# Kernel optimization log

Hardware: AMD Instinct MI355X
Metric: run time of the kernel (lower is better)

The kernel has to match this reference:

```python
import jax, jax.numpy as jnp
import numpy as np

N_NODES = 50000
N_EDGES = 800000
N_GRAPHS = 2500
HIDDEN = 64
IN_DIM = 14  # 11 QM9 features + 3 pos


def setup_inputs() -> dict:
    key = jax.random.key(0)
    ks = jax.random.split(key, 12)
    def glorot(k, shape):
        fan_in = shape[0]
        return jax.random.normal(k, shape, dtype=jnp.float32) / np.sqrt(fan_in)
    return {
        "x": jax.random.normal(ks[0], (N_NODES, 11), dtype=jnp.float32),
        "pos": jax.random.normal(ks[1], (N_NODES, 3), dtype=jnp.float32),
        "edge_index": jax.random.randint(ks[2], (2, N_EDGES), 0, N_NODES, dtype=jnp.int64),
        "batch": jnp.sort(jax.random.randint(ks[3], (N_NODES,), 0, N_GRAPHS, dtype=jnp.int64)),
        "W1a": glorot(ks[4], (IN_DIM, HIDDEN)),
        "b1a": jnp.zeros((HIDDEN,), jnp.float32),
        "W1b": glorot(ks[5], (HIDDEN, HIDDEN)),
        "b1b": jnp.zeros((HIDDEN,), jnp.float32),
        "W2a": glorot(ks[6], (HIDDEN, HIDDEN)),
        "b2a": jnp.zeros((HIDDEN,), jnp.float32),
        "W2b": glorot(ks[7], (HIDDEN, HIDDEN)),
        "b2b": jnp.zeros((HIDDEN,), jnp.float32),
        "Wlin": glorot(ks[8], (HIDDEN, 1)),
        "blin": jnp.zeros((1,), jnp.float32),
    }


def reference(x, pos, edge_index, batch, W1a, b1a, W1b, b1b, W2a, b2a, W2b, b2b, Wlin, blin):
    n = x.shape[0]
    src, dst = edge_index[0], edge_index[1]

    def gin_conv(h, Wa, ba, Wb, bb):
        # GINConv (eps=0): nn((1+eps)*h + sum_{j in N(i)} h_j)
        agg = jax.ops.segment_sum(h[src], dst, num_segments=n)  # scatter-add over edges
        z = h + agg
        return jax.nn.relu(z @ Wa + ba) @ Wb + bb

    h = jnp.concatenate([x, pos], axis=1)  # [N, 14]
    h = jax.nn.relu(gin_conv(h, W1a, b1a, W1b, b1b))
    h = jax.nn.relu(gin_conv(h, W2a, b2a, W2b, b2b))

    # global_mean_pool over graph ids
    sums = jax.ops.segment_sum(h, batch, num_segments=N_GRAPHS)            # [G, H]
    counts = jax.ops.segment_sum(jnp.ones((n,), h.dtype), batch, num_segments=N_GRAPHS)
    pooled = sums / jnp.maximum(counts, 1.0)[:, None]
    return pooled @ Wlin + blin  # [G, 1]
```

## Files before the change

kernel.cpp:

```cpp
#include <hip/hip_runtime.h>
#include <hip/hip_fp16.h>


typedef unsigned int uint;
typedef _Float16 half8 __attribute__((ext_vector_type(8)));
typedef float f32x4 __attribute__((ext_vector_type(4)));

#define BSH   6
#define NBKMAX 1024
#define EPB   2048
#define CAPSH 11
#define CAP   (1 << CAPSH)
#define ZBLK  64

__device__ __forceinline__ void addu(float* a, uint d) {
    __half2 h = *(__half2*)&d;
    a[0] += __low2float(h);
    a[1] += __high2float(h);
}
__device__ __forceinline__ half8 as_half8(uint4 u) {
    union { uint4 u; half8 h; } x; x.u = u; return x.h;
}


__global__ __launch_bounds__(256) void pack_bin(
    const float* __restrict__ x, const float* __restrict__ pos,
    uint2* __restrict__ xp2,
    const int* __restrict__ src, const int* __restrict__ dst,
    int* __restrict__ bkt_cnt, int* __restrict__ deg,
    uint* __restrict__ pairs,
    const float* __restrict__ W1a, const float* __restrict__ W1b,
    const float* __restrict__ W2a, const float* __restrict__ W2b,
    _Float16* __restrict__ wp1a, _Float16* __restrict__ wp1b,
    _Float16* __restrict__ wp2a, _Float16* __restrict__ wp2b,
    uint4* __restrict__ zbuf, int nz4,
    int packb, int nbk, int N, int E)
{
    int bx = (int)blockIdx.x;
    if (bx < ZBLK) {
        uint4 z4 = {0u, 0u, 0u, 0u};
        for (int idx = bx * 256 + threadIdx.x; idx < nz4; idx += ZBLK * 256)
            zbuf[idx] = z4;
        return;
    }
    bx -= ZBLK;
    if (bx == 0) {
        for (int idx = threadIdx.x; idx < 64 * 32; idx += 256) {
            int n = idx >> 5, k = idx & 31;
            wp1a[idx] = (k < 14) ? (_Float16)W1a[k * 64 + n] : (_Float16)0.f;
        }
        for (int idx = threadIdx.x; idx < 64 * 64; idx += 256) {
            int n = idx >> 6, k = idx & 63;
            wp1b[idx] = (_Float16)W1b[k * 64 + n];
            wp2a[idx] = (_Float16)W2a[k * 64 + n];
            wp2b[idx] = (_Float16)W2b[k * 64 + n];
        }
        return;
    }
    bx -= 1;
    if (bx < packb) {
        int i = bx * 256 + threadIdx.x;
        if (i >= N) return;
        float v[16];
#pragma unroll
        for (int k = 0; k < 11; k++) v[k] = x[(size_t)i * 11 + k];
        v[11] = pos[(size_t)i * 3 + 0];
        v[12] = pos[(size_t)i * 3 + 1];
        v[13] = pos[(size_t)i * 3 + 2];
        v[14] = 0.f; v[15] = 0.f;
#pragma unroll
        for (int c = 0; c < 4; c++) {
            __half2 l = __floats2half2_rn(v[4 * c],     v[4 * c + 1]);
            __half2 h = __floats2half2_rn(v[4 * c + 2], v[4 * c + 3]);
            uint2 u;
            u.x = *(uint*)&l;
            u.y = *(uint*)&h;
            xp2[(size_t)i * 4 + c] = u;
        }
        return;
    }
    bx -= packb;
    __shared__ int lcnt[NBKMAX];
    __shared__ int lbase[NBKMAX];
    for (int i = threadIdx.x; i < nbk; i += 256) lcnt[i] = 0;
    __syncthreads();
    int e0 = bx * EPB + threadIdx.x;
    uint pv[EPB / 256];
    int  rk[EPB / 256], bk[EPB / 256];
#pragma unroll
    for (int j = 0; j < EPB / 256; j++) {
        int e = e0 + j * 256;
        bk[j] = -1;
        if (e < E) {
            int s = src[e];
            int d = dst[e];
            bk[j] = d >> BSH;
            pv[j] = ((uint)(d & ((1 << BSH) - 1)) << 16) | (uint)s;
            rk[j] = atomicAdd(&lcnt[bk[j]], 1);
            atomicAdd(&deg[d], 1);
        }
    }
    __syncthreads();
    for (int i = threadIdx.x; i < nbk; i += 256) {
        int c = lcnt[i];
        lbase[i] = c ? atomicAdd(&bkt_cnt[i], c) : 0;
    }
    __syncthreads();
#pragma unroll
    for (int j = 0; j < EPB / 256; j++) {
        if (bk[j] >= 0) {
            int p = lbase[bk[j]] + rk[j];
            if (p < CAP)
                pairs[((size_t)bk[j] << CAPSH) + p] = pv[j];
        }
    }
}


__global__ __launch_bounds__(256) void bucket_build(
    const uint* __restrict__ pairs, const int* __restrict__ bkt_cnt,
    const int* __restrict__ deg,
    int* __restrict__ offs, int* __restrict__ ssrc, int N)
{
    __shared__ int cur[64];
    int b = blockIdx.x;
    int nbase = b << BSH;
    int nn = min(1 << BSH, N - nbase);
    int tid = threadIdx.x;
    int start = b << CAPSH;
    if (tid < 64) {
        int v = (tid < nn) ? deg[nbase + tid] : 0;
        int s = v;
#pragma unroll
        for (int off2 = 1; off2 < 64; off2 <<= 1) {
            int t = __shfl_up(s, off2, 64);
            if (tid >= off2) s += t;
        }
        int gofs = start + s - v;
        if (tid < nn) offs[nbase + tid] = gofs;
        cur[tid] = gofs;
    }
    __syncthreads();
    int end = start + min(bkt_cnt[b], CAP);
    for (int e = start + tid; e < end; e += 256) {
        uint pr = pairs[e];
        int p = atomicAdd(&cur[pr >> 16], 1);
        ssrc[p] = (int)(pr & 0xffffu);
    }
}


__global__ __launch_bounds__(256) void gather1_mlp1(
    const uint2* __restrict__ xp2,
    const int* __restrict__ offs, const int* __restrict__ deg,
    const int* __restrict__ ssrc,
    const _Float16* __restrict__ wp1a, const _Float16* __restrict__ wp1b,
    const float* __restrict__ b1a, const float* __restrict__ b1b,
    uint* __restrict__ h1p)
{
    __shared__ uint4 zb[16 * 2];
    __shared__ float hb[16 * 68];
    int lane = threadIdx.x & 63;
    int wid  = threadIdx.x >> 6;
    int i0 = blockIdx.x << 4;
    int n0 = i0 + wid * 4;

    int stv = 0, lnv = 0;
    if (lane < 4) { stv = offs[n0 + lane]; lnv = deg[n0 + lane]; }
    int n  = lane >> 4;
    int s  = (lane >> 2) & 3;
    int c  = lane & 3;
    int dn = __shfl(lnv, n, 64);
    int st = __shfl(stv, n, 64);
    int pA = lane & 15;
    int svA = 0, svB = 0;
    if (dn > 0)  svA = ssrc[st + min(pA, dn - 1)];
    if (dn > 16) svB = ssrc[st + min(16 + pA, dn - 1)];
    uint2 S = {0u, 0u};
    if (s == 0) S = xp2[(size_t)(n0 + n) * 4 + c];

    float a[4] = {0.f, 0.f, 0.f, 0.f};
#pragma unroll
    for (int it = 0; it < 4; ++it) {
        int pos = it * 4 + s;
        int sA = __shfl(svA, (n << 4) | pos, 64);
        if (pos < dn) {
            uint2 A = xp2[(size_t)sA * 4 + c];
            addu(a + 0, A.x); addu(a + 2, A.y);
        }
    }
    if (__any(dn > 16)) {
#pragma unroll
        for (int it = 4; it < 8; ++it) {
            int pos = it * 4 + s;
            int sB = __shfl(svB, (n << 4) | (pos - 16), 64);
            if (pos < dn) {
                uint2 A = xp2[(size_t)sB * 4 + c];
                addu(a + 0, A.x); addu(a + 2, A.y);
            }
        }
        int pos2 = 32 + s;
        while (__any(pos2 < dn)) {
            if (pos2 < dn) {
                int sid = ssrc[st + pos2];
                uint2 A = xp2[(size_t)sid * 4 + c];
                addu(a + 0, A.x); addu(a + 2, A.y);
            }
            pos2 += 4;
        }
    }
#pragma unroll
    for (int mm = 4; mm <= 8; mm <<= 1)
#pragma unroll
        for (int d = 0; d < 4; d++) a[d] += __shfl_xor(a[d], mm, 64);
    if (s == 0) {
        addu(a + 0, S.x); addu(a + 2, S.y);
        __half2 l  = __floats2half2_rn(a[0], a[1]);
        __half2 hh = __floats2half2_rn(a[2], a[3]);
        uint2 u;
        u.x = *(uint*)&l;
        u.y = *(uint*)&hh;
        ((uint2*)zb)[(wid * 4 + n) * 4 + c] = u;
    }
    __syncthreads();

    int m = lane & 15, quad = lane >> 4;
    int half = lane >> 5, p = lane & 31;
    int nw = wid * 16 + m;
    half8 BA  = *(const half8*)(wp1a + (size_t)nw * 32 + quad * 8);
    half8 BB0 = *(const half8*)(wp1b + (size_t)nw * 64 + quad * 8);
    half8 BB1 = *(const half8*)(wp1b + (size_t)nw * 64 + 32 + quad * 8);
    float baw = b1a[nw], bbw = b1b[nw];

    half8 A0;
#pragma unroll
    for (int jj = 0; jj < 8; jj++) A0[jj] = (_Float16)0.f;
    if (quad < 2)
        A0 = as_half8(zb[m * 2 + quad]);
    f32x4 acc = (f32x4){baw, baw, baw, baw};
    acc = __builtin_amdgcn_mfma_f32_16x16x32_f16(A0, BA, acc, 0, 0, 0);
#pragma unroll
    for (int r = 0; r < 4; r++)
        hb[(quad * 4 + r) * 68 + wid * 16 + m] = fmaxf(acc[r], 0.f);
    __syncthreads();
    half8 A1[2];
#pragma unroll
    for (int hh = 0; hh < 2; hh++)
#pragma unroll
        for (int jj = 0; jj < 8; jj++)
            A1[hh][jj] = (_Float16)hb[m * 68 + hh * 32 + quad * 8 + jj];
    f32x4 acc2 = (f32x4){bbw, bbw, bbw, bbw};
    acc2 = __builtin_amdgcn_mfma_f32_16x16x32_f16(A1[0], BB0, acc2, 0, 0, 0);
    acc2 = __builtin_amdgcn_mfma_f32_16x16x32_f16(A1[1], BB1, acc2, 0, 0, 0);
    __syncthreads();
#pragma unroll
    for (int r = 0; r < 4; r++)
        hb[(quad * 4 + r) * 68 + wid * 16 + m] = fmaxf(acc2[r], 0.f);
    __syncthreads();
#pragma unroll
    for (int it = 0; it < 2; it++) {
        int row = wid * 4 + it * 2 + half;
        float lo = hb[row * 68 + 2 * p];
        float hi = hb[row * 68 + 2 * p + 1];
        __half2 hh2 = __floats2half2_rn(lo, hi);
        h1p[(size_t)(i0 + row) * 32 + p] = *(uint*)&hh2;
    }
}


__global__ __launch_bounds__(256) void gather2_mlp2pool(
    const uint4* __restrict__ h4,
    const int* __restrict__ offs, const int* __restrict__ deg,
    const int* __restrict__ ssrc,
    const _Float16* __restrict__ wp2a, const _Float16* __restrict__ wp2b,
    const float* __restrict__ b2a, const float* __restrict__ b2b,
    const int* __restrict__ batch,
    float* __restrict__ sums, float* __restrict__ counts)
{
    __shared__ uint4 zb[16 * 8];
    __shared__ float hb[16 * 68];
    int lane = threadIdx.x & 63;
    int wid  = threadIdx.x >> 6;
    int i0 = blockIdx.x << 4;
    int n0 = i0 + wid * 4;

    int stv = 0, lnv = 0;
    if (lane < 4) { stv = offs[n0 + lane]; lnv = deg[n0 + lane]; }
    int n  = lane >> 4;
    int s  = (lane >> 3) & 1;
    int q  = lane & 7;
    int dn = __shfl(lnv, n, 64);
    int st = __shfl(stv, n, 64);
    int pA = lane & 15;
    int svA = 0, svB = 0;
    if (dn > 0)  svA = ssrc[st + min(pA, dn - 1)];
    if (dn > 16) svB = ssrc[st + min(16 + pA, dn - 1)];
    uint4 S = {0u, 0u, 0u, 0u};
    if (s == 0) S = h4[(size_t)(n0 + n) * 8 + q];

    float a[8] = {0.f, 0.f, 0.f, 0.f, 0.f, 0.f, 0.f, 0.f};
#pragma unroll
    for (int it = 0; it < 8; ++it) {
        int pos = it * 2 + s;
        int sA = __shfl(svA, (n << 4) | pos, 64);
        if (pos < dn) {
            uint4 A = h4[(size_t)sA * 8 + q];
            addu(a + 0, A.x); addu(a + 2, A.y); addu(a + 4, A.z); addu(a + 6, A.w);
        }
    }
    if (__any(dn > 16)) {
#pragma unroll
        for (int it = 8; it < 16; ++it) {
            int pos = it * 2 + s;
            int sB = __shfl(svB, (n << 4) | (pos - 16), 64);
            if (pos < dn) {
                uint4 A = h4[(size_t)sB * 8 + q];
                addu(a + 0, A.x); addu(a + 2, A.y); addu(a + 4, A.z); addu(a + 6, A.w);
            }
        }
        int pos2 = 32 + s;
        while (__any(pos2 < dn)) {
            if (pos2 < dn) {
                int sid = ssrc[st + pos2];
                uint4 A = h4[(size_t)sid * 8 + q];
                addu(a + 0, A.x); addu(a + 2, A.y); addu(a + 4, A.z); addu(a + 6, A.w);
            }
            pos2 += 2;
        }
    }
#pragma unroll
    for (int d = 0; d < 8; d++) a[d] += __shfl_xor(a[d], 8, 64);
    if (s == 0) {
        addu(a + 0, S.x); addu(a + 2, S.y); addu(a + 4, S.z); addu(a + 6, S.w);
        __half2 p0 = __floats2half2_rn(a[0], a[1]);
        __half2 p1 = __floats2half2_rn(a[2], a[3]);
        __half2 p2 = __floats2half2_rn(a[4], a[5]);
        __half2 p3 = __floats2half2_rn(a[6], a[7]);
        uint4 o4;
        o4.x = *(uint*)&p0; o4.y = *(uint*)&p1;
        o4.z = *(uint*)&p2; o4.w = *(uint*)&p3;
        zb[(wid * 4 + n) * 8 + q] = o4;
    }
    __syncthreads();

    int m = lane & 15, quad = lane >> 4;
    int nw = wid * 16 + m;
    half8 BA0 = *(const half8*)(wp2a + (size_t)nw * 64 + quad * 8);
    half8 BA1 = *(const half8*)(wp2a + (size_t)nw * 64 + 32 + quad * 8);
    half8 BB0 = *(const half8*)(wp2b + (size_t)nw * 64 + quad * 8);
    half8 BB1 = *(const half8*)(wp2b + (size_t)nw * 64 + 32 + quad * 8);
    float baw = b2a[nw], bbw = b2b[nw];

    half8 A0[2];
#pragma unroll
    for (int hh = 0; hh < 2; hh++)
        A0[hh] = as_half8(zb[m * 8 + hh * 4 + quad]);
    f32x4 acc = (f32x4){baw, baw, baw, baw};
    acc = __builtin_amdgcn_mfma_f32_16x16x32_f16(A0[0], BA0, acc, 0, 0, 0);
    acc = __builtin_amdgcn_mfma_f32_16x16x32_f16(A0[1], BA1, acc, 0, 0, 0);
#pragma unroll
    for (int r = 0; r < 4; r++)
        hb[(quad * 4 + r) * 68 + wid * 16 + m] = fmaxf(acc[r], 0.f);
    __syncthreads();
    half8 A1[2];
#pragma unroll
    for (int hh = 0; hh < 2; hh++)
#pragma unroll
        for (int jj = 0; jj < 8; jj++)
            A1[hh][jj] = (_Float16)hb[m * 68 + hh * 32 + quad * 8 + jj];
    f32x4 acc2 = (f32x4){bbw, bbw, bbw, bbw};
    acc2 = __builtin_amdgcn_mfma_f32_16x16x32_f16(A1[0], BB0, acc2, 0, 0, 0);
    acc2 = __builtin_amdgcn_mfma_f32_16x16x32_f16(A1[1], BB1, acc2, 0, 0, 0);
    __syncthreads();
#pragma unroll
    for (int r = 0; r < 4; r++)
        hb[(quad * 4 + r) * 68 + wid * 16 + m] = fmaxf(acc2[r], 0.f);
    __syncthreads();

    int gcur = batch[i0 + wid * 4]; float ps = 0.f; int cntn = 0;
#pragma unroll
    for (int nn = 0; nn < 4; nn++) {
        int row = wid * 4 + nn;
        float v = hb[row * 68 + lane];
        int gi = batch[i0 + row];
        if (gi != gcur) {
            atomicAdd(&sums[gcur * 64 + lane], ps);
            if (lane == 0) atomicAdd(&counts[gcur], (float)cntn);
            gcur = gi; ps = 0.f; cntn = 0;
        }
        ps += v; cntn++;
    }
    atomicAdd(&sums[gcur * 64 + lane], ps);
    if (lane == 0) atomicAdd(&counts[gcur], (float)cntn);
}

__global__ __launch_bounds__(256) void gin_final(
    const float* __restrict__ sums, const float* __restrict__ counts,
    const float* __restrict__ Wlin, const float* __restrict__ blin,
    float* __restrict__ out, int G)
{
    int lane = threadIdx.x & 63;
    int g    = blockIdx.x * 4 + (threadIdx.x >> 6);
    if (g < G) {
        float v = sums[g * 64 + lane] * Wlin[lane];
#pragma unroll
        for (int off = 32; off > 0; off >>= 1) v += __shfl_down(v, off, 64);
        if (lane == 0) out[g] = v / fmaxf(counts[g], 1.0f) + blin[0];
    }
}

extern "C" void kernel_launch(void* const* d_in, const int* in_sizes, int n_in,
                              void* d_out, int out_size, void* d_ws, size_t ws_size,
                              hipStream_t stream) {
    const float* x    = (const float*)d_in[0];
    const float* pos  = (const float*)d_in[1];
    const int*   ei   = (const int*)d_in[2];
    const int*   batch= (const int*)d_in[3];
    const float* W1a  = (const float*)d_in[4];
    const float* b1a  = (const float*)d_in[5];
    const float* W1b  = (const float*)d_in[6];
    const float* b1b  = (const float*)d_in[7];
    const float* W2a  = (const float*)d_in[8];
    const float* b2a  = (const float*)d_in[9];
    const float* W2b  = (const float*)d_in[10];
    const float* b2b  = (const float*)d_in[11];
    const float* Wlin = (const float*)d_in[12];
    const float* blin = (const float*)d_in[13];
    float* out = (float*)d_out;

    const int N = in_sizes[0] / 11;
    const int E = in_sizes[2] / 2;
    const int G = out_size;

    const int* src = ei;
    const int* dst = ei + E;
    const int nbk   = (N + (1 << BSH) - 1) >> BSH;
    const int packb = (N + 255) / 256;
    const int neb   = (E + EPB - 1) / EPB;
    const int NG    = N >> 4;

    char* ws = (char*)d_ws;
    size_t o = 0;
    float* sums    = (float*)(ws + o); o += (size_t)G * 64 * 4;
    float* counts  = (float*)(ws + o); o += (((size_t)G + 63) & ~(size_t)63) * 4;
    const int nz4  = (int)(((size_t)G * 64 + (((size_t)G + 63) & ~(size_t)63)) / 4);
    int*   bkt_cnt = (int*)(ws + o);   o += NBKMAX * 4;
    int*   deg     = (int*)(ws + o);   o += (size_t)N * 4;
    o = (o + 255) & ~(size_t)255;
    _Float16* wp1a = (_Float16*)(ws + o); o += 64 * 32 * 2;
    o = (o + 255) & ~(size_t)255;
    _Float16* wp1b = (_Float16*)(ws + o); o += 64 * 64 * 2;
    o = (o + 255) & ~(size_t)255;
    _Float16* wp2a = (_Float16*)(ws + o); o += 64 * 64 * 2;
    o = (o + 255) & ~(size_t)255;
    _Float16* wp2b = (_Float16*)(ws + o); o += 64 * 64 * 2;
    o = (o + 255) & ~(size_t)255;
    int*   offs    = (int*)(ws + o);   o += (size_t)N * 4;
    o = (o + 255) & ~(size_t)255;
    int*   ssrc    = (int*)(ws + o);   o += ((size_t)nbk << CAPSH) * 4;
    o = (o + 255) & ~(size_t)255;
    uint*  h1p     = (uint*)(ws + o);  o += (size_t)N * 32 * 4;
    o = (o + 255) & ~(size_t)255;
    uint2* xp2     = (uint2*)(ws + o); o += (size_t)N * 32;
    o = (o + 255) & ~(size_t)255;
    uint*  pairs   = (uint*)(ws + o);  o += ((size_t)nbk << CAPSH) * 4;

    hipMemsetAsync(bkt_cnt, 0, NBKMAX * 4 + (size_t)N * 4, stream);

    pack_bin<<<ZBLK + 1 + packb + neb, 256, 0, stream>>>(
        x, pos, xp2, src, dst, bkt_cnt, deg, pairs,
        W1a, W1b, W2a, W2b, wp1a, wp1b, wp2a, wp2b,
        (uint4*)sums, nz4, packb, nbk, N, E);
    bucket_build<<<nbk, 256, 0, stream>>>(pairs, bkt_cnt, deg, offs, ssrc, N);
    gather1_mlp1<<<NG, 256, 0, stream>>>(
        xp2, offs, deg, ssrc, wp1a, wp1b, b1a, b1b, h1p);
    gather2_mlp2pool<<<NG, 256, 0, stream>>>(
        (const uint4*)h1p, offs, deg, ssrc, wp2a, wp2b, b2a, b2b,
        batch, sums, counts);
    gin_final<<<(G + 3) / 4, 256, 0, stream>>>(
        sums, counts, Wlin, blin, out, G);
}
```

Before: 180.9 us.

## Replace CSR build with per-bucket LDS atomic scatter fused into MLP kernels

Removes the degree counting, per-node offset scan and sorted-source (ssrc) build. Each block now owns a 64-node destination bucket, walks its unsorted pairs list and accumulates neighbor features into fp32 shared memory with LDS atomics, then runs the MLP on those 64 rows. This drops one kernel launch, the deg atomics and the memset of deg, plus the ssrc/offs global traffic. In exchange it adds LDS atomic contention, uses fewer and larger blocks (782 instead of 3125), and raises EPB to 4096.

```diff
diff --git a/kernel.cpp b/kernel.cpp
--- a/kernel.cpp
+++ b/kernel.cpp
@@ -8,16 +8,11 @@
 
 #define BSH   6
 #define NBKMAX 1024
-#define EPB   2048
+#define EPB   4096
 #define CAPSH 11
 #define CAP   (1 << CAPSH)
 #define ZBLK  64
 
-__device__ __forceinline__ void addu(float* a, uint d) {
-    __half2 h = *(__half2*)&d;
-    a[0] += __low2float(h);
-    a[1] += __high2float(h);
-}
 __device__ __forceinline__ half8 as_half8(uint4 u) {
     union { uint4 u; half8 h; } x; x.u = u; return x.h;
 }
@@ -27,8 +22,7 @@
     const float* __restrict__ x, const float* __restrict__ pos,
     uint2* __restrict__ xp2,
     const int* __restrict__ src, const int* __restrict__ dst,
-    int* __restrict__ bkt_cnt, int* __restrict__ deg,
-    uint* __restrict__ pairs,
+    int* __restrict__ bkt_cnt, uint* __restrict__ pairs,
     const float* __restrict__ W1a, const float* __restrict__ W1b,
     const float* __restrict__ W2a, const float* __restrict__ W2b,
     _Float16* __restrict__ wp1a, _Float16* __restrict__ wp1b,
@@ -97,7 +91,6 @@
             bk[j] = d >> BSH;
             pv[j] = ((uint)(d & ((1 << BSH) - 1)) << 16) | (uint)s;
             rk[j] = atomicAdd(&lcnt[bk[j]], 1);
-            atomicAdd(&deg[d], 1);
         }
     }
     __syncthreads();
@@ -117,272 +110,226 @@
 }
 
 
-__global__ __launch_bounds__(256) void bucket_build(
+__global__ __launch_bounds__(256) void bucket_g1m1(
+    const uint* __restrict__ xp2u,
+    const uint2* __restrict__ xp2,
     const uint* __restrict__ pairs, const int* __restrict__ bkt_cnt,
-    const int* __restrict__ deg,
-    int* __restrict__ offs, int* __restrict__ ssrc, int N)
-{
-    __shared__ int cur[64];
-    int b = blockIdx.x;
-    int nbase = b << BSH;
-    int nn = min(1 << BSH, N - nbase);
-    int tid = threadIdx.x;
-    int start = b << CAPSH;
-    if (tid < 64) {
-        int v = (tid < nn) ? deg[nbase + tid] : 0;
-        int s = v;
-#pragma unroll
-        for (int off2 = 1; off2 < 64; off2 <<= 1) {
-            int t = __shfl_up(s, off2, 64);
-            if (tid >= off2) s += t;
-        }
-        int gofs = start + s - v;
-        if (tid < nn) offs[nbase + tid] = gofs;
-        cur[tid] = gofs;
-    }
-    __syncthreads();
-    int end = start + min(bkt_cnt[b], CAP);
-    for (int e = start + tid; e < end; e += 256) {
-        uint pr = pairs[e];
-        int p = atomicAdd(&cur[pr >> 16], 1);
-        ssrc[p] = (int)(pr & 0xffffu);
-    }
-}
-
-
-__global__ __launch_bounds__(256) void gather1_mlp1(
-    const uint2* __restrict__ xp2,
-    const int* __restrict__ offs, const int* __restrict__ deg,
-    const int* __restrict__ ssrc,
     const _Float16* __restrict__ wp1a, const _Float16* __restrict__ wp1b,
     const float* __restrict__ b1a, const float* __restrict__ b1b,
-    uint* __restrict__ h1p)
+    uint* __restrict__ h1p, int N)
 {
-    __shared__ uint4 zb[16 * 2];
-    __shared__ float hb[16 * 68];
-    int lane = threadIdx.x & 63;
-    int wid  = threadIdx.x >> 6;
-    int i0 = blockIdx.x << 4;
-    int n0 = i0 + wid * 4;
-
-    int stv = 0, lnv = 0;
-    if (lane < 4) { stv = offs[n0 + lane]; lnv = deg[n0 + lane]; }
-    int n  = lane >> 4;
-    int s  = (lane >> 2) & 3;
-    int c  = lane & 3;
-    int dn = __shfl(lnv, n, 64);
-    int st = __shfl(stv, n, 64);
-    int pA = lane & 15;
-    int svA = 0, svB = 0;
-    if (dn > 0)  svA = ssrc[st + min(pA, dn - 1)];
-    if (dn > 16) svB = ssrc[st + min(16 + pA, dn - 1)];
-    uint2 S = {0u, 0u};
-    if (s == 0) S = xp2[(size_t)(n0 + n) * 4 + c];
-
-    float a[4] = {0.f, 0.f, 0.f, 0.f};
-#pragma unroll
-    for (int it = 0; it < 4; ++it) {
-        int pos = it * 4 + s;
-        int sA = __shfl(svA, (n << 4) | pos, 64);
-        if (pos < dn) {
-            uint2 A = xp2[(size_t)sA * 4 + c];
-            addu(a + 0, A.x); addu(a + 2, A.y);
-        }
-    }
-    if (__any(dn > 16)) {
-#pragma unroll
-        for (int it = 4; it < 8; ++it) {
-            int pos = it * 4 + s;
-            int sB = __shfl(svB, (n << 4) | (pos - 16), 64);
-            if (pos < dn) {
-                uint2 A = xp2[(size_t)sB * 4 + c];
-                addu(a + 0, A.x); addu(a + 2, A.y);
-            }
-        }
-        int pos2 = 32 + s;
-        while (__any(pos2 < dn)) {
-            if (pos2 < dn) {
-                int sid = ssrc[st + pos2];
-                uint2 A = xp2[(size_t)sid * 4 + c];
-                addu(a + 0, A.x); addu(a + 2, A.y);
-            }
-            pos2 += 4;
-        }
-    }
-#pragma unroll
-    for (int mm = 4; mm <= 8; mm <<= 1)
-#pragma unroll
-        for (int d = 0; d < 4; d++) a[d] += __shfl_xor(a[d], mm, 64);
-    if (s == 0) {
-        addu(a + 0, S.x); addu(a + 2, S.y);
-        __half2 l  = __floats2half2_rn(a[0], a[1]);
-        __half2 hh = __floats2half2_rn(a[2], a[3]);
-        uint2 u;
-        u.x = *(uint*)&l;
-        u.y = *(uint*)&hh;
-        ((uint2*)zb)[(wid * 4 + n) * 4 + c] = u;
-    }
-    __syncthreads();
-
+    __shared__ float z[64 * 18];
+    __shared__ float hb[4][16 * 68];
+    int b = blockIdx.x;
+    int nbase = b << 6;
+    int tid = threadIdx.x;
+    int lane = tid & 63, wid = tid >> 6;
+
+    {
+        int n = tid >> 2, fq = tid & 3;
+        int node = nbase + n;
+        if (node < N) {
+            uint2 u = xp2[(size_t)node * 4 + fq];
+            __half2 h0 = *(__half2*)&u.x;
+            __half2 h1 = *(__half2*)&u.y;
+            float* zp = &z[n * 18 + fq * 4];
+            zp[0] = __low2float(h0); zp[1] = __high2float(h0);
+            zp[2] = __low2float(h1); zp[3] = __high2float(h1);
+        }
+    }
+    __syncthreads();
+
+    int start = b << CAPSH;
+    int end = start + min(bkt_cnt[b], CAP);
+    int fpart = tid & 7;
+    for (int e = start + (tid >> 3); e < end; e += 32) {
+        uint pr = pairs[e];
+        int s    = (int)(pr & 0xffffu);
+        int dloc = (int)(pr >> 16);
+        uint u = xp2u[(size_t)s * 8 + fpart];
+        __half2 h = *(__half2*)&u;
+        atomicAdd(&z[dloc * 18 + fpart * 2 + 0], __low2float(h));
+        atomicAdd(&z[dloc * 18 + fpart * 2 + 1], __high2float(h));
+    }
+    __syncthreads();
+
+    int row0 = nbase + wid * 16;
+    if (row0 >= N) return;
     int m = lane & 15, quad = lane >> 4;
-    int half = lane >> 5, p = lane & 31;
-    int nw = wid * 16 + m;
-    half8 BA  = *(const half8*)(wp1a + (size_t)nw * 32 + quad * 8);
-    half8 BB0 = *(const half8*)(wp1b + (size_t)nw * 64 + quad * 8);
-    half8 BB1 = *(const half8*)(wp1b + (size_t)nw * 64 + 32 + quad * 8);
-    float baw = b1a[nw], bbw = b1b[nw];
+    float* h = hb[wid];
+
+    half8 BA[4]; half8 BB[4][2];
+    float ba[4], bb[4];
+#pragma unroll
+    for (int t = 0; t < 4; t++) {
+        BA[t]    = *(const half8*)(wp1a + (size_t)(t * 16 + m) * 32 + quad * 8);
+        BB[t][0] = *(const half8*)(wp1b + (size_t)(t * 16 + m) * 64 + quad * 8);
+        BB[t][1] = *(const half8*)(wp1b + (size_t)(t * 16 + m) * 64 + 32 + quad * 8);
+        ba[t] = b1a[t * 16 + m];
+        bb[t] = b1b[t * 16 + m];
+    }
 
     half8 A0;
 #pragma unroll
     for (int jj = 0; jj < 8; jj++) A0[jj] = (_Float16)0.f;
-    if (quad < 2)
-        A0 = as_half8(zb[m * 2 + quad]);
-    f32x4 acc = (f32x4){baw, baw, baw, baw};
-    acc = __builtin_amdgcn_mfma_f32_16x16x32_f16(A0, BA, acc, 0, 0, 0);
-#pragma unroll
-    for (int r = 0; r < 4; r++)
-        hb[(quad * 4 + r) * 68 + wid * 16 + m] = fmaxf(acc[r], 0.f);
-    __syncthreads();
+    if (quad < 2) {
+        const float* zp = &z[(wid * 16 + m) * 18 + quad * 8];
+#pragma unroll
+        for (int jj = 0; jj < 8; jj++) A0[jj] = (_Float16)zp[jj];
+    }
+    f32x4 acc[4];
+#pragma unroll
+    for (int t = 0; t < 4; t++) {
+        acc[t] = (f32x4){ba[t], ba[t], ba[t], ba[t]};
+        acc[t] = __builtin_amdgcn_mfma_f32_16x16x32_f16(A0, BA[t], acc[t], 0, 0, 0);
+    }
+#pragma unroll
+    for (int t = 0; t < 4; t++)
+#pragma unroll
+        for (int r = 0; r < 4; r++)
+            h[(quad * 4 + r) * 68 + t * 16 + m] = fmaxf(acc[t][r], 0.f);
     half8 A1[2];
 #pragma unroll
     for (int hh = 0; hh < 2; hh++)
 #pragma unroll
         for (int jj = 0; jj < 8; jj++)
-            A1[hh][jj] = (_Float16)hb[m * 68 + hh * 32 + quad * 8 + jj];
-    f32x4 acc2 = (f32x4){bbw, bbw, bbw, bbw};
-    acc2 = __builtin_amdgcn_mfma_f32_16x16x32_f16(A1[0], BB0, acc2, 0, 0, 0);
-    acc2 = __builtin_amdgcn_mfma_f32_16x16x32_f16(A1[1], BB1, acc2, 0, 0, 0);
-    __syncthreads();
-#pragma unroll
-    for (int r = 0; r < 4; r++)
-        hb[(quad * 4 + r) * 68 + wid * 16 + m] = fmaxf(acc2[r], 0.f);
-    __syncthreads();
-#pragma unroll
-    for (int it = 0; it < 2; it++) {
-        int row = wid * 4 + it * 2 + half;
-        float lo = hb[row * 68 + 2 * p];
-        float hi = hb[row * 68 + 2 * p + 1];
+            A1[hh][jj] = (_Float16)h[m * 68 + hh * 32 + quad * 8 + jj];
+    f32x4 acc2[4];
+#pragma unroll
+    for (int t = 0; t < 4; t++) {
+        acc2[t] = (f32x4){bb[t], bb[t], bb[t], bb[t]};
+        acc2[t] = __builtin_amdgcn_mfma_f32_16x16x32_f16(A1[0], BB[t][0], acc2[t], 0, 0, 0);
+        acc2[t] = __builtin_amdgcn_mfma_f32_16x16x32_f16(A1[1], BB[t][1], acc2[t], 0, 0, 0);
+    }
+#pragma unroll
+    for (int t = 0; t < 4; t++)
+#pragma unroll
+        for (int r = 0; r < 4; r++)
+            h[(quad * 4 + r) * 68 + t * 16 + m] = fmaxf(acc2[t][r], 0.f);
+    int half_ = lane >> 5, p = lane & 31;
+#pragma unroll
+    for (int it = 0; it < 8; it++) {
+        int row = it * 2 + half_;
+        float lo = h[row * 68 + 2 * p];
+        float hi = h[row * 68 + 2 * p + 1];
         __half2 hh2 = __floats2half2_rn(lo, hi);
-        h1p[(size_t)(i0 + row) * 32 + p] = *(uint*)&hh2;
-    }
-}
-
-
-__global__ __launch_bounds__(256) void gather2_mlp2pool(
-    const uint4* __restrict__ h4,
-    const int* __restrict__ offs, const int* __restrict__ deg,
-    const int* __restrict__ ssrc,
+        h1p[(size_t)(row0 + row) * 32 + p] = *(uint*)&hh2;
+    }
+}
+
+
+__global__ __launch_bounds__(256) void bucket_g2m2pool(
+    const uint2* __restrict__ h1p2,
+    const uint4* __restrict__ h1p4,
+    const uint* __restrict__ pairs, const int* __restrict__ bkt_cnt,
     const _Float16* __restrict__ wp2a, const _Float16* __restrict__ wp2b,
     const float* __restrict__ b2a, const float* __restrict__ b2b,
     const int* __restrict__ batch,
-    float* __restrict__ sums, float* __restrict__ counts)
+    float* __restrict__ sums, float* __restrict__ counts, int N)
 {
-    __shared__ uint4 zb[16 * 8];
-    __shared__ float hb[16 * 68];
-    int lane = threadIdx.x & 63;
-    int wid  = threadIdx.x >> 6;
-    int i0 = blockIdx.x << 4;
-    int n0 = i0 + wid * 4;
-
-    int stv = 0, lnv = 0;
-    if (lane < 4) { stv = offs[n0 + lane]; lnv = deg[n0 + lane]; }
-    int n  = lane >> 4;
-    int s  = (lane >> 3) & 1;
-    int q  = lane & 7;
-    int dn = __shfl(lnv, n, 64);
-    int st = __shfl(stv, n, 64);
-    int pA = lane & 15;
-    int svA = 0, svB = 0;
-    if (dn > 0)  svA = ssrc[st + min(pA, dn - 1)];
-    if (dn > 16) svB = ssrc[st + min(16 + pA, dn - 1)];
-    uint4 S = {0u, 0u, 0u, 0u};
-    if (s == 0) S = h4[(size_t)(n0 + n) * 8 + q];
-
-    float a[8] = {0.f, 0.f, 0.f, 0.f, 0.f, 0.f, 0.f, 0.f};
-#pragma unroll
-    for (int it = 0; it < 8; ++it) {
-        int pos = it * 2 + s;
-        int sA = __shfl(svA, (n << 4) | pos, 64);
-        if (pos < dn) {
-            uint4 A = h4[(size_t)sA * 8 + q];
-            addu(a + 0, A.x); addu(a + 2, A.y); addu(a + 4, A.z); addu(a + 6, A.w);
-        }
-    }
-    if (__any(dn > 16)) {
-#pragma unroll
-        for (int it = 8; it < 16; ++it) {
-            int pos = it * 2 + s;
-            int sB = __shfl(svB, (n << 4) | (pos - 16), 64);
-            if (pos < dn) {
-                uint4 A = h4[(size_t)sB * 8 + q];
-                addu(a + 0, A.x); addu(a + 2, A.y); addu(a + 4, A.z); addu(a + 6, A.w);
+    __shared__ float z[64 * 66];
+    __shared__ float hb[4][16 * 68];
+    int b = blockIdx.x;
+    int nbase = b << 6;
+    int tid = threadIdx.x;
+    int lane = tid & 63, wid = tid >> 6;
+
+    {
+        int n = tid >> 2, pp = tid & 3;
+        int node = nbase + n;
+        if (node < N) {
+            uint4 ua = h1p4[(size_t)node * 8 + pp * 2];
+            uint4 ub = h1p4[(size_t)node * 8 + pp * 2 + 1];
+            float* zp = &z[n * 66 + pp * 16];
+            const uint uu[8] = {ua.x, ua.y, ua.z, ua.w, ub.x, ub.y, ub.z, ub.w};
+#pragma unroll
+            for (int k = 0; k < 8; k++) {
+                __half2 h = *(__half2*)&uu[k];
+                zp[2 * k]     = __low2float(h);
+                zp[2 * k + 1] = __high2float(h);
             }
         }
-        int pos2 = 32 + s;
-        while (__any(pos2 < dn)) {
-            if (pos2 < dn) {
-                int sid = ssrc[st + pos2];
-                uint4 A = h4[(size_t)sid * 8 + q];
-                addu(a + 0, A.x); addu(a + 2, A.y); addu(a + 4, A.z); addu(a + 6, A.w);
-            }
-            pos2 += 2;
-        }
-    }
-#pragma unroll
-    for (int d = 0; d < 8; d++) a[d] += __shfl_xor(a[d], 8, 64);
-    if (s == 0) {
-        addu(a + 0, S.x); addu(a + 2, S.y); addu(a + 4, S.z); addu(a + 6, S.w);
-        __half2 p0 = __floats2half2_rn(a[0], a[1]);
-        __half2 p1 = __floats2half2_rn(a[2], a[3]);
-        __half2 p2 = __floats2half2_rn(a[4], a[5]);
-        __half2 p3 = __floats2half2_rn(a[6], a[7]);
-        uint4 o4;
-        o4.x = *(uint*)&p0; o4.y = *(uint*)&p1;
-        o4.z = *(uint*)&p2; o4.w = *(uint*)&p3;
-        zb[(wid * 4 + n) * 8 + q] = o4;
-    }
-    __syncthreads();
-
+    }
+    __syncthreads();
+
+    int start = b << CAPSH;
+    int end = start + min(bkt_cnt[b], CAP);
+    int part = tid & 15;
+    for (int e = start + (tid >> 4); e < end; e += 16) {
+        uint pr = pairs[e];
+        int s    = (int)(pr & 0xffffu);
+        int dloc = (int)(pr >> 16);
+        uint2 u = h1p2[(size_t)s * 16 + part];
+        __half2 ha = *(__half2*)&u.x;
+        __half2 hbv = *(__half2*)&u.y;
+        float* zp = &z[dloc * 66 + part * 4];
+        atomicAdd(zp + 0, __low2float(ha));
+        atomicAdd(zp + 1, __high2float(ha));
+        atomicAdd(zp + 2, __low2float(hbv));
+        atomicAdd(zp + 3, __high2float(hbv));
+    }
+    __syncthreads();
+
+    int row0 = nbase + wid * 16;
+    if (row0 >= N) return;
     int m = lane & 15, quad = lane >> 4;
-    int nw = wid * 16 + m;
-    half8 BA0 = *(const half8*)(wp2a + (size_t)nw * 64 + quad * 8);
-    half8 BA1 = *(const half8*)(wp2a + (size_t)nw * 64 + 32 + quad * 8);
-    half8 BB0 = *(const half8*)(wp2b + (size_t)nw * 64 + quad * 8);
-    half8 BB1 = *(const half8*)(wp2b + (size_t)nw * 64 + 32 + quad * 8);
-    float baw = b2a[nw], bbw = b2b[nw];
+    float* h = hb[wid];
+
+    half8 BA[4][2], BB[4][2];
+    float ba[4], bb[4];
+#pragma unroll
+    for (int t = 0; t < 4; t++) {
+        BA[t][0] = *(const half8*)(wp2a + (size_t)(t * 16 + m) * 64 + quad * 8);
+        BA[t][1] = *(const half8*)(wp2a + (size_t)(t * 16 + m) * 64 + 32 + quad * 8);
+        BB[t][0] = *(const half8*)(wp2b + (size_t)(t * 16 + m) * 64 + quad * 8);
+        BB[t][1] = *(const half8*)(wp2b + (size_t)(t * 16 + m) * 64 + 32 + quad * 8);
+        ba[t] = b2a[t * 16 + m];
+        bb[t] = b2b[t * 16 + m];
+    }
 
     half8 A0[2];
 #pragma unroll
+    for (int hh = 0; hh < 2; hh++) {
+        const float* zp = &z[(wid * 16 + m) * 66 + hh * 32 + quad * 8];
+#pragma unroll
+        for (int jj = 0; jj < 8; jj++) A0[hh][jj] = (_Float16)zp[jj];
+    }
+    f32x4 acc[4];
+#pragma unroll
+    for (int t = 0; t < 4; t++) {
+        acc[t] = (f32x4){ba[t], ba[t], ba[t], ba[t]};
+        acc[t] = __builtin_amdgcn_mfma_f32_16x16x32_f16(A0[0], BA[t][0], acc[t], 0, 0, 0);
+        acc[t] = __builtin_amdgcn_mfma_f32_16x16x32_f16(A0[1], BA[t][1], acc[t], 0, 0, 0);
+    }
+#pragma unroll
+    for (int t = 0; t < 4; t++)
+#pragma unroll
+        for (int r = 0; r < 4; r++)
+            h[(quad * 4 + r) * 68 + t * 16 + m] = fmaxf(acc[t][r], 0.f);
+    half8 A1[2];
+#pragma unroll
     for (int hh = 0; hh < 2; hh++)
-        A0[hh] = as_half8(zb[m * 8 + hh * 4 + quad]);
-    f32x4 acc = (f32x4){baw, baw, baw, baw};
-    acc = __builtin_amdgcn_mfma_f32_16x16x32_f16(A0[0], BA0, acc, 0, 0, 0);
-    acc = __builtin_amdgcn_mfma_f32_16x16x32_f16(A0[1], BA1, acc, 0, 0, 0);
-#pragma unroll
-    for (int r = 0; r < 4; r++)
-        hb[(quad * 4 + r) * 68 + wid * 16 + m] = fmaxf(acc[r], 0.f);
-    __syncthreads();
-    half8 A1[2];
-#pragma unroll
-    for (int hh = 0; hh < 2; hh++)
 #pragma unroll
         for (int jj = 0; jj < 8; jj++)
-            A1[hh][jj] = (_Float16)hb[m * 68 + hh * 32 + quad * 8 + jj];
-    f32x4 acc2 = (f32x4){bbw, bbw, bbw, bbw};
-    acc2 = __builtin_amdgcn_mfma_f32_16x16x32_f16(A1[0], BB0, acc2, 0, 0, 0);
-    acc2 = __builtin_amdgcn_mfma_f32_16x16x32_f16(A1[1], BB1, acc2, 0, 0, 0);
-    __syncthreads();
-#pragma unroll
-    for (int r = 0; r < 4; r++)
-        hb[(quad * 4 + r) * 68 + wid * 16 + m] = fmaxf(acc2[r], 0.f);
-    __syncthreads();
-
-    int gcur = batch[i0 + wid * 4]; float ps = 0.f; int cntn = 0;
-#pragma unroll
-    for (int nn = 0; nn < 4; nn++) {
-        int row = wid * 4 + nn;
-        float v = hb[row * 68 + lane];
-        int gi = batch[i0 + row];
+            A1[hh][jj] = (_Float16)h[m * 68 + hh * 32 + quad * 8 + jj];
+    f32x4 acc2[4];
+#pragma unroll
+    for (int t = 0; t < 4; t++) {
+        acc2[t] = (f32x4){bb[t], bb[t], bb[t], bb[t]};
+        acc2[t] = __builtin_amdgcn_mfma_f32_16x16x32_f16(A1[0], BB[t][0], acc2[t], 0, 0, 0);
+        acc2[t] = __builtin_amdgcn_mfma_f32_16x16x32_f16(A1[1], BB[t][1], acc2[t], 0, 0, 0);
+    }
+#pragma unroll
+    for (int t = 0; t < 4; t++)
+#pragma unroll
+        for (int r = 0; r < 4; r++)
+            h[(quad * 4 + r) * 68 + t * 16 + m] = fmaxf(acc2[t][r], 0.f);
+
+    int gcur = batch[row0]; float ps = 0.f; int cntn = 0;
+#pragma unroll
+    for (int nn = 0; nn < 16; nn++) {
+        float v = h[nn * 68 + lane];
+        int gi = batch[row0 + nn];
         if (gi != gcur) {
             atomicAdd(&sums[gcur * 64 + lane], ps);
             if (lane == 0) atomicAdd(&counts[gcur], (float)cntn);
@@ -437,7 +384,6 @@
     const int nbk   = (N + (1 << BSH) - 1) >> BSH;
     const int packb = (N + 255) / 256;
     const int neb   = (E + EPB - 1) / EPB;
-    const int NG    = N >> 4;
 
     char* ws = (char*)d_ws;
     size_t o = 0;
@@ -445,7 +391,6 @@
     float* counts  = (float*)(ws + o); o += (((size_t)G + 63) & ~(size_t)63) * 4;
     const int nz4  = (int)(((size_t)G * 64 + (((size_t)G + 63) & ~(size_t)63)) / 4);
     int*   bkt_cnt = (int*)(ws + o);   o += NBKMAX * 4;
-    int*   deg     = (int*)(ws + o);   o += (size_t)N * 4;
     o = (o + 255) & ~(size_t)255;
     _Float16* wp1a = (_Float16*)(ws + o); o += 64 * 32 * 2;
     o = (o + 255) & ~(size_t)255;
@@ -455,28 +400,23 @@
     o = (o + 255) & ~(size_t)255;
     _Float16* wp2b = (_Float16*)(ws + o); o += 64 * 64 * 2;
     o = (o + 255) & ~(size_t)255;
-    int*   offs    = (int*)(ws + o);   o += (size_t)N * 4;
-    o = (o + 255) & ~(size_t)255;
-    int*   ssrc    = (int*)(ws + o);   o += ((size_t)nbk << CAPSH) * 4;
-    o = (o + 255) & ~(size_t)255;
     uint*  h1p     = (uint*)(ws + o);  o += (size_t)N * 32 * 4;
     o = (o + 255) & ~(size_t)255;
     uint2* xp2     = (uint2*)(ws + o); o += (size_t)N * 32;
     o = (o + 255) & ~(size_t)255;
     uint*  pairs   = (uint*)(ws + o);  o += ((size_t)nbk << CAPSH) * 4;
 
-    hipMemsetAsync(bkt_cnt, 0, NBKMAX * 4 + (size_t)N * 4, stream);
+    hipMemsetAsync(bkt_cnt, 0, NBKMAX * 4, stream);
 
     pack_bin<<<ZBLK + 1 + packb + neb, 256, 0, stream>>>(
-        x, pos, xp2, src, dst, bkt_cnt, deg, pairs,
+        x, pos, xp2, src, dst, bkt_cnt, pairs,
         W1a, W1b, W2a, W2b, wp1a, wp1b, wp2a, wp2b,
         (uint4*)sums, nz4, packb, nbk, N, E);
-    bucket_build<<<nbk, 256, 0, stream>>>(pairs, bkt_cnt, deg, offs, ssrc, N);
-    gather1_mlp1<<<NG, 256, 0, stream>>>(
-        xp2, offs, deg, ssrc, wp1a, wp1b, b1a, b1b, h1p);
-    gather2_mlp2pool<<<NG, 256, 0, stream>>>(
-        (const uint4*)h1p, offs, deg, ssrc, wp2a, wp2b, b2a, b2b,
-        batch, sums, counts);
+    bucket_g1m1<<<nbk, 256, 0, stream>>>(
+        (const uint*)xp2, xp2, pairs, bkt_cnt, wp1a, wp1b, b1a, b1b, h1p, N);
+    bucket_g2m2pool<<<nbk, 256, 0, stream>>>(
+        (const uint2*)h1p, (const uint4*)h1p, pairs, bkt_cnt,
+        wp2a, wp2b, b2a, b2b, batch, sums, counts, N);
     gin_final<<<(G + 3) / 4, 256, 0, stream>>>(
         sums, counts, Wlin, blin, out, G);
 }
```

Measured after the change: 540.1 us. +198.5%, slower.

## Compute node degrees from bucket pairs instead of global atomics; vectorize edge binning

Applied to the files above, without the earlier changes.

Removes the per-edge global atomicAdd on deg during binning. Degrees are now counted with LDS atomics inside bucket_build, which keeps the bucket's pairs in registers for both the count and the scatter passes. Edge binning now handles 4096 edges per block, each thread loading 16 contiguous edges with int4 loads, and the deg memset is dropped. The trade-off is more registers per thread and fewer binning blocks. The fixed 8-per-thread register load in bucket_build only covers buckets up to CAP entries, which is the same cap as before.

```diff
diff --git a/kernel.cpp b/kernel.cpp
--- a/kernel.cpp
+++ b/kernel.cpp
@@ -8,7 +8,7 @@
 
 #define BSH   6
 #define NBKMAX 1024
-#define EPB   2048
+#define EPB   4096
 #define CAPSH 11
 #define CAP   (1 << CAPSH)
 #define ZBLK  64
@@ -27,8 +27,7 @@
     const float* __restrict__ x, const float* __restrict__ pos,
     uint2* __restrict__ xp2,
     const int* __restrict__ src, const int* __restrict__ dst,
-    int* __restrict__ bkt_cnt, int* __restrict__ deg,
-    uint* __restrict__ pairs,
+    int* __restrict__ bkt_cnt, uint* __restrict__ pairs,
     const float* __restrict__ W1a, const float* __restrict__ W1b,
     const float* __restrict__ W2a, const float* __restrict__ W2b,
     _Float16* __restrict__ wp1a, _Float16* __restrict__ wp1b,
@@ -82,32 +81,56 @@
     bx -= packb;
     __shared__ int lcnt[NBKMAX];
     __shared__ int lbase[NBKMAX];
-    for (int i = threadIdx.x; i < nbk; i += 256) lcnt[i] = 0;
-    __syncthreads();
-    int e0 = bx * EPB + threadIdx.x;
-    uint pv[EPB / 256];
-    int  rk[EPB / 256], bk[EPB / 256];
-#pragma unroll
-    for (int j = 0; j < EPB / 256; j++) {
-        int e = e0 + j * 256;
-        bk[j] = -1;
-        if (e < E) {
-            int s = src[e];
-            int d = dst[e];
-            bk[j] = d >> BSH;
-            pv[j] = ((uint)(d & ((1 << BSH) - 1)) << 16) | (uint)s;
+    int tid = threadIdx.x;
+    for (int i = tid; i < nbk; i += 256) lcnt[i] = 0;
+    __syncthreads();
+    int eb = bx * EPB;
+    uint pv[16];
+    int  rk[16], bk[16];
+    if (eb + EPB <= E) {
+        const int4* s4 = (const int4*)(src + eb) + tid * 4;
+        const int4* d4 = (const int4*)(dst + eb) + tid * 4;
+        int4 sv[4], dv[4];
+#pragma unroll
+        for (int g = 0; g < 4; g++) { sv[g] = s4[g]; dv[g] = d4[g]; }
+#pragma unroll
+        for (int g = 0; g < 4; g++) {
+            int ss[4] = {sv[g].x, sv[g].y, sv[g].z, sv[g].w};
+            int dd[4] = {dv[g].x, dv[g].y, dv[g].z, dv[g].w};
+#pragma unroll
+            for (int k = 0; k < 4; k++) {
+                int j = g * 4 + k;
+                bk[j] = dd[k] >> BSH;
+                pv[j] = ((uint)(dd[k] & ((1 << BSH) - 1)) << 16) | (uint)ss[k];
+            }
+        }
+#pragma unroll
+        for (int j = 0; j < 16; j++)
             rk[j] = atomicAdd(&lcnt[bk[j]], 1);
-            atomicAdd(&deg[d], 1);
-        }
-    }
-    __syncthreads();
-    for (int i = threadIdx.x; i < nbk; i += 256) {
+    } else {
+#pragma unroll
+        for (int j = 0; j < 16; j++) {
+            int e = eb + tid * 16 + j;
+            bk[j] = -1;
+            if (e < E) {
+                int s = src[e];
+                int d = dst[e];
+                bk[j] = d >> BSH;
+                pv[j] = ((uint)(d & ((1 << BSH) - 1)) << 16) | (uint)s;
+            }
+        }
+#pragma unroll
+        for (int j = 0; j < 16; j++)
+            if (bk[j] >= 0) rk[j] = atomicAdd(&lcnt[bk[j]], 1);
+    }
+    __syncthreads();
+    for (int i = tid; i < nbk; i += 256) {
         int c = lcnt[i];
         lbase[i] = c ? atomicAdd(&bkt_cnt[i], c) : 0;
     }
     __syncthreads();
 #pragma unroll
-    for (int j = 0; j < EPB / 256; j++) {
+    for (int j = 0; j < 16; j++) {
         if (bk[j] >= 0) {
             int p = lbase[bk[j]] + rk[j];
             if (p < CAP)
@@ -119,34 +142,51 @@
 
 __global__ __launch_bounds__(256) void bucket_build(
     const uint* __restrict__ pairs, const int* __restrict__ bkt_cnt,
-    const int* __restrict__ deg,
-    int* __restrict__ offs, int* __restrict__ ssrc, int N)
+    int* __restrict__ offs, int* __restrict__ deg,
+    int* __restrict__ ssrc, int N)
 {
+    __shared__ int cnt[64];
     __shared__ int cur[64];
     int b = blockIdx.x;
     int nbase = b << BSH;
     int nn = min(1 << BSH, N - nbase);
     int tid = threadIdx.x;
+    if (tid < 64) cnt[tid] = 0;
+    __syncthreads();
     int start = b << CAPSH;
+    int cntE = min(bkt_cnt[b], CAP);
+    uint pr[8];
+#pragma unroll
+    for (int k = 0; k < 8; k++) {
+        int e = tid + k * 256;
+        pr[k] = (e < cntE) ? pairs[start + e] : 0xffffffffu;
+    }
+#pragma unroll
+    for (int k = 0; k < 8; k++)
+        if (pr[k] != 0xffffffffu) atomicAdd(&cnt[pr[k] >> 16], 1);
+    __syncthreads();
     if (tid < 64) {
-        int v = (tid < nn) ? deg[nbase + tid] : 0;
+        int v = cnt[tid];
         int s = v;
 #pragma unroll
-        for (int off2 = 1; off2 < 64; off2 <<= 1) {
-            int t = __shfl_up(s, off2, 64);
-            if (tid >= off2) s += t;
+        for (int o2 = 1; o2 < 64; o2 <<= 1) {
+            int t = __shfl_up(s, o2, 64);
+            if (tid >= o2) s += t;
         }
         int gofs = start + s - v;
-        if (tid < nn) offs[nbase + tid] = gofs;
+        if (tid < nn) {
+            offs[nbase + tid] = gofs;
+            deg[nbase + tid]  = v;
+        }
         cur[tid] = gofs;
     }
     __syncthreads();
-    int end = start + min(bkt_cnt[b], CAP);
-    for (int e = start + tid; e < end; e += 256) {
-        uint pr = pairs[e];
-        int p = atomicAdd(&cur[pr >> 16], 1);
-        ssrc[p] = (int)(pr & 0xffffu);
-    }
+#pragma unroll
+    for (int k = 0; k < 8; k++)
+        if (pr[k] != 0xffffffffu) {
+            int p = atomicAdd(&cur[pr[k] >> 16], 1);
+            ssrc[p] = (int)(pr[k] & 0xffffu);
+        }
 }
 
 
@@ -445,18 +485,18 @@
     float* counts  = (float*)(ws + o); o += (((size_t)G + 63) & ~(size_t)63) * 4;
     const int nz4  = (int)(((size_t)G * 64 + (((size_t)G + 63) & ~(size_t)63)) / 4);
     int*   bkt_cnt = (int*)(ws + o);   o += NBKMAX * 4;
+    o = (o + 255) & ~(size_t)255;
+    _Float16* wp1a = (_Float16*)(ws + o); o += 64 * 32 * 2;
+    o = (o + 255) & ~(size_t)255;
+    _Float16* wp1b = (_Float16*)(ws + o); o += 64 * 64 * 2;
+    o = (o + 255) & ~(size_t)255;
+    _Float16* wp2a = (_Float16*)(ws + o); o += 64 * 64 * 2;
+    o = (o + 255) & ~(size_t)255;
+    _Float16* wp2b = (_Float16*)(ws + o); o += 64 * 64 * 2;
+    o = (o + 255) & ~(size_t)255;
+    int*   offs    = (int*)(ws + o);   o += (size_t)N * 4;
     int*   deg     = (int*)(ws + o);   o += (size_t)N * 4;
     o = (o + 255) & ~(size_t)255;
-    _Float16* wp1a = (_Float16*)(ws + o); o += 64 * 32 * 2;
-    o = (o + 255) & ~(size_t)255;
-    _Float16* wp1b = (_Float16*)(ws + o); o += 64 * 64 * 2;
-    o = (o + 255) & ~(size_t)255;
-    _Float16* wp2a = (_Float16*)(ws + o); o += 64 * 64 * 2;
-    o = (o + 255) & ~(size_t)255;
-    _Float16* wp2b = (_Float16*)(ws + o); o += 64 * 64 * 2;
-    o = (o + 255) & ~(size_t)255;
-    int*   offs    = (int*)(ws + o);   o += (size_t)N * 4;
-    o = (o + 255) & ~(size_t)255;
     int*   ssrc    = (int*)(ws + o);   o += ((size_t)nbk << CAPSH) * 4;
     o = (o + 255) & ~(size_t)255;
     uint*  h1p     = (uint*)(ws + o);  o += (size_t)N * 32 * 4;
@@ -465,13 +505,13 @@
     o = (o + 255) & ~(size_t)255;
     uint*  pairs   = (uint*)(ws + o);  o += ((size_t)nbk << CAPSH) * 4;
 
-    hipMemsetAsync(bkt_cnt, 0, NBKMAX * 4 + (size_t)N * 4, stream);
+    hipMemsetAsync(bkt_cnt, 0, NBKMAX * 4, stream);
 
     pack_bin<<<ZBLK + 1 + packb + neb, 256, 0, stream>>>(
-        x, pos, xp2, src, dst, bkt_cnt, deg, pairs,
+        x, pos, xp2, src, dst, bkt_cnt, pairs,
         W1a, W1b, W2a, W2b, wp1a, wp1b, wp2a, wp2b,
         (uint4*)sums, nz4, packb, nbk, N, E);
-    bucket_build<<<nbk, 256, 0, stream>>>(pairs, bkt_cnt, deg, offs, ssrc, N);
+    bucket_build<<<nbk, 256, 0, stream>>>(pairs, bkt_cnt, offs, deg, ssrc, N);
     gather1_mlp1<<<NG, 256, 0, stream>>>(
         xp2, offs, deg, ssrc, wp1a, wp1b, b1a, b1b, h1p);
     gather2_mlp2pool<<<NG, 256, 0, stream>>>(
```

After: 148.3 us (median of 2 runs). 18.0% less time.
